# Kernel optimization log

Hardware: AMD Instinct MI355X
Metric: run time of the kernel (lower is better)

## Reference

```python
import jax, jax.numpy as jnp
import numpy as np
from jax.scipy.special import gammaln, xlogy

B, N, DIM, H, DK, DV = 2, 2048, 1536, 8, 64, 64
NRPF = 192  # num_rel_pos_features, already divisible by 6


def get_positional_embed(n, feat):
    # Enformer positional basis: exponential, central-mask, gamma; then sign-antisymmetrized.
    nb = feat // 6  # num basis per class
    d = jnp.arange(-n + 1, n, dtype=jnp.float32)          # [2n-1]
    ad = jnp.abs(d)[:, None]                              # [2n-1, 1]
    # exponential decay features
    max_range = np.log(n) / np.log(2.0)
    half_life = 2.0 ** jnp.linspace(3.0, max_range, nb)
    e = jnp.exp(-np.log(2.0) / half_life * ad)
    # central mask features
    widths = 2.0 ** jnp.arange(1, nb + 1, dtype=jnp.float32) - 1.0
    c = (widths > ad).astype(jnp.float32)
    # gamma pdf features
    std = n / (2.0 * nb)
    mean = jnp.linspace(n / nb, float(n), nb)
    conc = (mean / std) ** 2
    rate = mean / (std ** 2)
    logp = xlogy(conc - 1.0, ad) - rate * ad - (gammaln(conc) - conc * jnp.log(rate))
    p = jnp.exp(logp) + 1e-8
    g = p / jnp.max(p)
    emb = jnp.concatenate([e, c, g], axis=-1)             # [2n-1, feat//2]
    return jnp.concatenate([emb, jnp.sign(d)[:, None] * emb], axis=-1)  # [2n-1, feat]


def relative_shift(x):
    # x: [b, h, i, 2i-1] -> [b, h, i, i]
    b, h, i, j = x.shape
    x = jnp.pad(x, ((0, 0), (0, 0), (0, 0), (1, 0)))      # [b,h,i,j+1]
    x = x.reshape(b, h, j + 1, i)[:, :, 1:, :]            # drop first 'row'
    x = x.reshape(b, h, i, j)
    return x[..., : (j + 2) // 2]                          # keep first i cols


def setup_inputs() -> dict:
    key = jax.random.key(0)
    ks = jax.random.split(key, 9)
    s = 0.02
    return {
        "x": jax.random.normal(ks[0], (B, N, DIM), jnp.float32),
        "Wq": jax.random.normal(ks[1], (DIM, H * DK), jnp.float32) * s,
        "Wk": jax.random.normal(ks[2], (DIM, H * DK), jnp.float32) * s,
        "Wv": jax.random.normal(ks[3], (DIM, H * DV), jnp.float32) * s,
        "Wo": jax.random.normal(ks[4], (H * DV, DIM), jnp.float32) * s,
        "bo": jnp.zeros((DIM,), jnp.float32),
        "Wrel": jax.random.normal(ks[5], (NRPF, H * DK), jnp.float32) * s,
        "rel_content_bias": jax.random.normal(ks[6], (1, H, 1, DK), jnp.float32),
        "rel_pos_bias": jax.random.normal(ks[7], (1, H, 1, DK), jnp.float32),
    }


def reference(x, Wq, Wk, Wv, Wo, bo, Wrel, rel_content_bias, rel_pos_bias):
    b, n, _ = x.shape
    scale = DK ** -0.5
    split = lambda t, d: t.reshape(b, n, H, d).transpose(0, 2, 1, 3)  # b h n d
    q = split(x @ Wq, DK) * scale
    k = split(x @ Wk, DK)
    v = split(x @ Wv, DV)
    content_logits = jnp.einsum('bhid,bhjd->bhij', q + rel_content_bias, k)
    pos = get_positional_embed(n, NRPF) @ Wrel               # [2n-1, H*DK]
    pos = pos.reshape(2 * n - 1, H, DK).transpose(1, 0, 2)   # h j d
    rel_logits = jnp.einsum('bhid,hjd->bhij', q + rel_pos_bias, pos)
    rel_logits = relative_shift(rel_logits)
    attn = jax.nn.softmax(content_logits + rel_logits, axis=-1)
    out = jnp.einsum('bhij,bhjd->bhid', attn, v)
    out = out.transpose(0, 2, 1, 3).reshape(b, n, H * DV)
    return out @ Wo + bo
```

## Files before the change

kernel.cpp:

```cpp
#include <hip/hip_runtime.h>
#include <stdint.h>
#include <cmath>

#define B_    2
#define N_    2048
#define DIM_  1536
#define H_    8
#define NPOS  (2*N_ - 1)
#define NB_   32

typedef __attribute__((ext_vector_type(8))) short short8;
typedef __attribute__((ext_vector_type(4))) float float4v;

struct PosConsts {
    float  inv_hl[32];
    int    widthI[32];
    float  c1[32];
    float  rateF[32];
    double gc[32];
    double maxp;
};

__device__ __forceinline__ float bf2f(unsigned short u) {
    return __uint_as_float(((unsigned int)u) << 16);
}
__device__ __forceinline__ unsigned short f2bf(float f) {
    unsigned int u = __float_as_uint(f);
    u += 0x7FFFu + ((u >> 16) & 1u);
    return (unsigned short)(u >> 16);
}
__device__ __forceinline__ unsigned int cvtpk(float lo, float hi) {
    unsigned int r;
    asm("v_cvt_pk_bf16_f32 %0, %1, %2" : "=v"(r) : "v"(lo), "v"(hi));
    return r;
}
__device__ __forceinline__ unsigned int pack2bf(float lo, float hi) {
    return cvtpk(lo, hi);
}
__device__ __forceinline__ float ldf(const void* p, int isF32, size_t idx) {
    return isF32 ? ((const float*)p)[idx] : bf2f(((const unsigned short*)p)[idx]);
}
__device__ __forceinline__ void gll16(const unsigned short* g, unsigned short* l) {
    __builtin_amdgcn_global_load_lds(
        (const __attribute__((address_space(1))) unsigned int*)g,
        (__attribute__((address_space(3))) unsigned int*)l, 16, 0, 0);
}

constexpr size_t OFF_FLAG = 0;
constexpr size_t OFF_POS  = 256;
constexpr size_t OFF_Q    = OFF_POS + (size_t)H_*4096*64*2;
constexpr size_t OFF_K    = OFF_Q   + (size_t)B_*H_*N_*64*2;
constexpr size_t OFF_V    = OFF_K   + (size_t)B_*H_*N_*64*2;
constexpr size_t OFF_WOT  = OFF_V   + (size_t)B_*H_*N_*64*2;
constexpr size_t OFF_XB   = OFF_WOT + (size_t)DIM_*512*2;
constexpr size_t OFF_AO   = OFF_XB;
constexpr size_t OFF_OP   = OFF_AO + (size_t)4096*512*2;
constexpr size_t OFF_LP   = OFF_OP + (size_t)3*16*32*4096*2;
constexpr size_t OFF_WT   = OFF_XB + (size_t)4096*DIM_*2;
static_assert(OFF_LP + (size_t)3*16*32*64*4 <= OFF_WT + (size_t)3*512*DIM_*2, "ws overflow");

__global__ __launch_bounds__(512) void prep_kernel(PosConsts pc,
                                                   const void* __restrict__ x,
                                                   const void* __restrict__ Wq, const void* __restrict__ Wk,
                                                   const void* __restrict__ Wv, const void* __restrict__ Wo,
                                                   const void* __restrict__ Wrel,
                                                   unsigned int* __restrict__ flags,
                                                   unsigned short* __restrict__ Xb,
                                                   unsigned short* __restrict__ Wt,
                                                   unsigned short* __restrict__ Wot,
                                                   unsigned short* __restrict__ posb) {
    __shared__ __align__(16) char smraw[16 * 192 * 4];
    const int tid = threadIdx.x;
    const int bid = blockIdx.x;

    int* cnt = (int*)smraw;
    int ok = 0;
    if (tid < 256) {
        unsigned short u = ((const unsigned short*)x)[2 * tid];
        int e = (u >> 7) & 0xFF;
        ok = (u == 0) || (e >= 95 && e <= 140);
    }
    cnt[tid] = ok;
    __syncthreads();
    for (int s = 256; s > 0; s >>= 1) {
        if (tid < s) cnt[tid] += cnt[tid + s];
        __syncthreads();
    }
    const int f32 = !(cnt[0] >= 192);
    __syncthreads();
    if (bid == 0 && tid == 0) flags[0] = (unsigned int)f32;

    if (bid < 256) {
        float* eb = (float*)smraw;
        const int j0 = bid * 16;
        const int c  = tid;
        for (int u = c; u < 16 * 96; u += 512) {
            int rr = u / 96, f = u - rr * 96;
            int j = j0 + rr;
            float v = 0.f, sg = 0.f;
            if (j < NPOS) {
                int dd  = j - (N_ - 1);
                int adI = dd < 0 ? -dd : dd;
                float val;
                if (f < 32) {
                    val = exp2f(-(float)adI * pc.inv_hl[f]);
                } else if (f < 64) {
                    val = (adI < pc.widthI[f - 32]) ? 1.f : 0.f;
                } else {
                    int g = f - 64;
                    if (adI == 0) {
                        val = (float)(1e-8 / pc.maxp);
                    } else {
                        double lp = (double)pc.c1[g] * log((double)adI)
                                  - (double)pc.rateF[g] * (double)adI + pc.gc[g];
                        double p = (double)expf((float)lp) + 1e-8;
                        val = (float)(p / pc.maxp);
                    }
                }
                v  = val;
                sg = (dd > 0) ? 1.f : ((dd < 0) ? -1.f : 0.f);
            }
            eb[rr * 192 + f]      = v;
            eb[rr * 192 + 96 + f] = sg * v;
        }
        __syncthreads();
        float acc[16];
#pragma unroll
        for (int rr = 0; rr < 16; ++rr) acc[rr] = 0.f;
        for (int k = 0; k < 192; k += 4) {
            float w0 = ldf(Wrel, f32, (size_t)(k + 0) * 512 + c);
            float w1 = ldf(Wrel, f32, (size_t)(k + 1) * 512 + c);
            float w2 = ldf(Wrel, f32, (size_t)(k + 2) * 512 + c);
            float w3 = ldf(Wrel, f32, (size_t)(k + 3) * 512 + c);
#pragma unroll
            for (int rr = 0; rr < 16; ++rr) {
                float4v e = *reinterpret_cast<const float4v*>(&eb[rr * 192 + k]);
                acc[rr] += e[0] * w0;
                acc[rr] += e[1] * w1;
                acc[rr] += e[2] * w2;
                acc[rr] += e[3] * w3;
            }
        }
        int h = c >> 6, dcol = c & 63;
#pragma unroll
        for (int rr = 0; rr < 16; ++rr) {
            int j = j0 + rr;
            if (j < NPOS)
                posb[((size_t)h * 4096 + j) * 64 + (dcol ^ ((j & 7) << 3))] = f2bf(acc[rr]);
        }
    } else if (bid < 1024) {
        unsigned short (*tile)[66] = (unsigned short(*)[66])smraw;
        const int idx = bid - 256;
        const int z = idx / 192, rem = idx % 192;
        const void* src = z == 0 ? Wq : (z == 1 ? Wk : (z == 2 ? Wv : Wo));
        unsigned short* dst = (z < 3) ? (Wt + (size_t)z * 512 * DIM_) : Wot;
        const int C     = (z < 3) ? 512 : DIM_;
        const int Rrows = (z < 3) ? DIM_ : 512;
        const int xt = C >> 6;
        const int bx = rem % xt, by = rem / xt;
        const int x0 = bx * 64, y0 = by * 64;
        const int tx2 = tid & 63, ty2 = tid >> 6;
#pragma unroll
        for (int i = 0; i < 8; ++i)
            tile[ty2 + i * 8][tx2] = f2bf(ldf(src, f32, (size_t)(y0 + ty2 + i * 8) * C + x0 + tx2));
        __syncthreads();
#pragma unroll
        for (int i = 0; i < 8; ++i)
            dst[(size_t)(x0 + ty2 + i * 8) * Rrows + y0 + tx2] = tile[tx2][ty2 + i * 8];
    } else {
        const int ab = bid - 1024;
        const size_t total = (size_t)4096 * DIM_;
        size_t i = ((size_t)ab * 512 + tid) * 8;
        const size_t stride = (size_t)1024 * 512 * 8;
        if (f32) {
            for (; i < total; i += stride) {
                float4v a = *reinterpret_cast<const float4v*>((const float*)x + i);
                float4v b = *reinterpret_cast<const float4v*>((const float*)x + i + 4);
                uint4 o;
                o.x = pack2bf(a[0], a[1]); o.y = pack2bf(a[2], a[3]);
                o.z = pack2bf(b[0], b[1]); o.w = pack2bf(b[2], b[3]);
                *reinterpret_cast<uint4*>(Xb + i) = o;
            }
        } else {
            for (; i < total; i += stride)
                *reinterpret_cast<uint4*>(Xb + i) =
                    *reinterpret_cast<const uint4*>((const unsigned short*)x + i);
        }
    }
}

__device__ __forceinline__ void gemm64x128_core(const unsigned short* __restrict__ A,
                                                const unsigned short* __restrict__ Bt,
                                                int K, int row0, int col0,
                                                unsigned short* As, unsigned short* Bs,
                                                float4v acc[2][4]) {
    const int tid = threadIdx.x, lane = tid & 63, w = tid >> 6;
    const int l15 = lane & 15, q8 = (lane >> 4) * 8;
    const int mr0 = (w & 1) * 32, nc0 = (w >> 1) * 64;
    const int sr = lane >> 2, sc8 = (lane & 3) * 8;
    for (int k0 = 0; k0 < K; k0 += 32) {
        __syncthreads();
        gll16(&A [(size_t)(row0 + w * 16 + sr) * K + k0 + sc8],      &As[w * 512]);
        gll16(&Bt[(size_t)(col0 + w * 32 + sr) * K + k0 + sc8],      &Bs[w * 1024]);
        gll16(&Bt[(size_t)(col0 + w * 32 + 16 + sr) * K + k0 + sc8], &Bs[w * 1024 + 512]);
        __syncthreads();
        short8 a[2], b[4];
#pragma unroll
        for (int mi = 0; mi < 2; ++mi)
            a[mi] = *reinterpret_cast<const short8*>(&As[(mr0 + mi * 16 + l15) * 32 + q8]);
#pragma unroll
        for (int ni = 0; ni < 4; ++ni)
            b[ni] = *reinterpret_cast<const short8*>(&Bs[(nc0 + ni * 16 + l15) * 32 + q8]);
#pragma unroll
        for (int mi = 0; mi < 2; ++mi)
#pragma unroll
            for (int ni = 0; ni < 4; ++ni)
                acc[mi][ni] = __builtin_amdgcn_mfma_f32_16x16x32_bf16(a[mi], b[ni], acc[mi][ni], 0, 0, 0);
    }
}

__global__ __launch_bounds__(256) void qkv_kernel(const unsigned short* __restrict__ Xb,
                                                  const unsigned short* __restrict__ Wt,
                                                  unsigned short* __restrict__ qbuf,
                                                  unsigned short* __restrict__ kbuf,
                                                  unsigned short* __restrict__ vbuf) {
    __shared__ __align__(16) unsigned short smem[64 * 32 + 128 * 32];
    unsigned short* As = smem;
    unsigned short* Bs = smem + 64 * 32;
    const int row0 = blockIdx.y * 64, col0 = blockIdx.x * 128;
    float4v acc[2][4];
#pragma unroll
    for (int mi = 0; mi < 2; ++mi)
#pragma unroll
        for (int ni = 0; ni < 4; ++ni) acc[mi][ni] = (float4v){0.f, 0.f, 0.f, 0.f};
    gemm64x128_core(Xb, Wt, DIM_, row0, col0, As, Bs, acc);
    __syncthreads();

    const int lane = threadIdx.x & 63, w = threadIdx.x >> 6;
    const int l15 = lane & 15, quad = lane >> 4;
    const int mr0 = (w & 1) * 32, nc0 = (w >> 1) * 64;
    const int n0 = col0 + nc0;
    const int mode = n0 >> 9;
    const int hh = (n0 & 511) >> 6;

    if (mode == 2) {
#pragma unroll
        for (int mi = 0; mi < 2; ++mi)
#pragma unroll
            for (int ni = 0; ni < 4; ++ni) {
                int dd = ni * 16 + l15;
                int mb = row0 + mr0 + mi * 16 + quad * 4;
                int bb = mb >> 11, ii = mb & 2047;
                union { unsigned short us[4]; uint2 u2; } pk;
                unsigned int p0 = cvtpk(acc[mi][ni][0], acc[mi][ni][1]);
                unsigned int p1 = cvtpk(acc[mi][ni][2], acc[mi][ni][3]);
                pk.u2 = (uint2){p0, p1};
                int jb = (ii & ~63) | ((ii & 63) ^ ((dd & 7) << 3));
                *reinterpret_cast<uint2*>(
                    &vbuf[((size_t)(bb * 8 + hh) * 64 + dd) * 2048 + jb]) = pk.u2;
            }
    } else {
        unsigned short* Obuf = (mode == 0) ? qbuf : kbuf;
        const float scale = (mode == 0) ? 0.125f : 1.0f;
        unsigned short* Lw = smem + w * 16 * 72;
        const int r16 = lane >> 2, c4 = (lane & 3) * 16;
#pragma unroll
        for (int mi = 0; mi < 2; ++mi) {
#pragma unroll
            for (int ni = 0; ni < 4; ++ni)
#pragma unroll
                for (int r = 0; r < 4; ++r)
                    Lw[(quad * 4 + r) * 72 + ni * 16 + l15] = f2bf(acc[mi][ni][r] * scale);
            int mb = row0 + mr0 + mi * 16 + r16;
            int bb = mb >> 11, tok = mb & 2047;
            unsigned short* gp = &Obuf[((size_t)(bb * 8 + hh) * N_ + tok) * 64];
            uint4 v0 = *reinterpret_cast<const uint4*>(&Lw[r16 * 72 + c4]);
            uint4 v1 = *reinterpret_cast<const uint4*>(&Lw[r16 * 72 + c4 + 8]);
            int swz2 = (mode == 1) ? ((tok & 7) << 3) : 0;
            *reinterpret_cast<uint4*>(gp + (c4 ^ swz2))       = v0;
            *reinterpret_cast<uint4*>(gp + ((c4 + 8) ^ swz2)) = v1;
        }
    }
}

#define SLD 72
#define RST 68

__device__ __forceinline__ void stage_lin(const unsigned short* __restrict__ g,
                                          unsigned short* s, int tid, int w) {
    gll16(g + tid * 8,        s + w * 512);
    gll16(g + 2048 + tid * 8, s + 2048 + w * 512);
}
__device__ __forceinline__ void stage_vt(const unsigned short* __restrict__ vbase,
                                         int jbase, unsigned short* s, int tid, int w) {
    {
        int L = tid * 8;        int d = L >> 6, cb = L & 63;
        gll16(vbase + (size_t)d * 2048 + jbase + cb, s + w * 512);
    }
    {
        int L = 2048 + tid * 8; int d = L >> 6, cb = L & 63;
        gll16(vbase + (size_t)d * 2048 + jbase + cb, s + 2048 + w * 512);
    }
}

__global__ __launch_bounds__(256) void attn_kernel(const unsigned int* __restrict__ flags,
                                                   const unsigned short* __restrict__ qb,
                                                   const unsigned short* __restrict__ kb,
                                                   const unsigned short* __restrict__ vb,
                                                   const unsigned short* __restrict__ posb,
                                                   const void* __restrict__ rcb,
                                                   const void* __restrict__ rpb,
                                                   unsigned short* __restrict__ ao) {
    __shared__ __align__(16) unsigned short Ks[2][4096];
    __shared__ __align__(16) unsigned short Ps[2][4096];
    __shared__ __align__(16) unsigned short Vt[2][4096];
    __shared__ __align__(16) unsigned short Pp[64 * SLD];
    __shared__ __align__(8)  unsigned short Rb[128 * RST];

    const int f32 = (int)flags[0];
    const int tid = threadIdx.x;
    const int it = blockIdx.x, bh = blockIdx.y;
    const int h = bh & 7, b = bh >> 3;
    const int i0 = it * 64;
    const size_t qoff = (size_t)bh * N_ * 64;
    const size_t poff = (size_t)h * 4096 * 64;
    const unsigned short* vbase = vb + (size_t)bh * 64 * 2048;
    const int lane = tid & 63, w = tid >> 6;
    const int l15 = lane & 15, quad = lane >> 4, q8 = quad * 8;
    const int m0 = w * 16 + quad * 4;
    const int swz = (l15 & 7) << 3;

    short8 afc[2], afr[2];
#pragma unroll
    for (int kc = 0; kc < 2; ++kc) {
        uint4 qv = *reinterpret_cast<const uint4*>(
            &qb[qoff + (size_t)(i0 + w * 16 + l15) * 64 + kc * 32 + q8]);
        unsigned int uu[4] = {qv.x, qv.y, qv.z, qv.w};
        unsigned int cw[4], rw[4];
#pragma unroll
        for (int e = 0; e < 4; ++e) {
            int k = h * 64 + kc * 32 + q8 + 2 * e;
            float lo = __uint_as_float(uu[e] << 16);
            float hi = __uint_as_float(uu[e] & 0xffff0000u);
            cw[e] = pack2bf(lo + ldf(rcb, f32, k), hi + ldf(rcb, f32, k + 1));
            rw[e] = pack2bf(lo + ldf(rpb, f32, k), hi + ldf(rpb, f32, k + 1));
        }
        union { uint4 u; short8 s; } cv, rv2;
        cv.u  = (uint4){cw[0], cw[1], cw[2], cw[3]};
        rv2.u = (uint4){rw[0], rw[1], rw[2], rw[3]};
        afc[kc] = cv.s;
        afr[kc] = rv2.s;
    }

    float4v Oa[4];
#pragma unroll
    for (int nb = 0; nb < 4; ++nb) Oa[nb] = (float4v){0.f, 0.f, 0.f, 0.f};
    float lsum[4] = {0.f, 0.f, 0.f, 0.f};

    const int base0 = 1984 - i0;
    const int NT = 32;
    const int cs0 = base0;

    {
        int r = tid >> 2, c16 = (tid & 3) * 16;
        const uint4* psrc = reinterpret_cast<const uint4*>(&posb[poff + (size_t)(cs0 + r) * 64 + c16]);
        *reinterpret_cast<uint4*>(&Ps[0][r * 64 + c16])     = psrc[0];
        *reinterpret_cast<uint4*>(&Ps[0][r * 64 + c16 + 8]) = psrc[1];
    }
    __syncthreads();
    {
        float4v R[4];
#pragma unroll
        for (int nb = 0; nb < 4; ++nb) R[nb] = (float4v){0.f, 0.f, 0.f, 0.f};
        __builtin_amdgcn_s_setprio(1);
#pragma unroll
        for (int kc = 0; kc < 2; ++kc)
#pragma unroll
            for (int nb = 0; nb < 4; ++nb) {
                short8 pb = *reinterpret_cast<const short8*>(
                    &Ps[0][(nb * 16 + l15) * 64 + ((kc * 32 + q8) ^ swz)]);
                R[nb] = __builtin_amdgcn_mfma_f32_16x16x32_bf16(afr[kc], pb, R[nb], 0, 0, 0);
            }
        __builtin_amdgcn_s_setprio(0);
#pragma unroll
        for (int nb = 0; nb < 4; ++nb) {
            int ta = cs0 + nb * 16 + l15;
            unsigned int pk0 = cvtpk(R[nb][0], R[nb][1]);
            unsigned int pk1 = cvtpk(R[nb][2], R[nb][3]);
            Rb[(size_t)((ta + m0 + 0) & 127) * RST + m0 + 0] = (unsigned short)pk0;
            Rb[(size_t)((ta + m0 + 1) & 127) * RST + m0 + 1] = (unsigned short)(pk0 >> 16);
            Rb[(size_t)((ta + m0 + 2) & 127) * RST + m0 + 2] = (unsigned short)pk1;
            Rb[(size_t)((ta + m0 + 3) & 127) * RST + m0 + 3] = (unsigned short)(pk1 >> 16);
        }
    }
    __syncthreads();

    stage_lin(&kb[qoff], Ks[0], tid, w);
    stage_lin(&posb[poff + (size_t)(cs0 + 64) * 64], Ps[0], tid, w);
    stage_vt(vbase, 0, Vt[0], tid, w);

    for (int u = 0; u < NT; ++u) {
        const int p = u & 1;
        const int j0 = u * 64, basej = base0 + j0;
        __syncthreads();

        if (u + 1 < NT) {
            stage_lin(&kb[qoff + (size_t)(j0 + 64) * 64], Ks[p ^ 1], tid, w);
            stage_lin(&posb[poff + (size_t)(cs0 + (u + 2) * 64) * 64], Ps[p ^ 1], tid, w);
            stage_vt(vbase, j0 + 64, Vt[p ^ 1], tid, w);
        }

        {
            float4v R[4];
#pragma unroll
            for (int nb = 0; nb < 4; ++nb) R[nb] = (float4v){0.f, 0.f, 0.f, 0.f};
            __builtin_amdgcn_s_setprio(1);
#pragma unroll
            for (int kc = 0; kc < 2; ++kc)
#pragma unroll
                for (int nb = 0; nb < 4; ++nb) {
                    short8 pb = *reinterpret_cast<const short8*>(
                        &Ps[p][(nb * 16 + l15) * 64 + ((kc * 32 + q8) ^ swz)]);
                    R[nb] = __builtin_amdgcn_mfma_f32_16x16x32_bf16(afr[kc], pb, R[nb], 0, 0, 0);
                }
            __builtin_amdgcn_s_setprio(0);
            const int tb = basej + 64;
#pragma unroll
            for (int nb = 0; nb < 4; ++nb) {
                int ta = tb + nb * 16 + l15;
                unsigned int pk0 = cvtpk(R[nb][0], R[nb][1]);
                unsigned int pk1 = cvtpk(R[nb][2], R[nb][3]);
                Rb[(size_t)((ta + m0 + 0) & 127) * RST + m0 + 0] = (unsigned short)pk0;
                Rb[(size_t)((ta + m0 + 1) & 127) * RST + m0 + 1] = (unsigned short)(pk0 >> 16);
                Rb[(size_t)((ta + m0 + 2) & 127) * RST + m0 + 2] = (unsigned short)pk1;
                Rb[(size_t)((ta + m0 + 3) & 127) * RST + m0 + 3] = (unsigned short)(pk1 >> 16);
            }
        }

        float4v Sacc[4];
#pragma unroll
        for (int nb = 0; nb < 4; ++nb) Sacc[nb] = (float4v){0.f, 0.f, 0.f, 0.f};
        __builtin_amdgcn_s_setprio(1);
#pragma unroll
        for (int kc = 0; kc < 2; ++kc)
#pragma unroll
            for (int nb = 0; nb < 4; ++nb) {
                short8 kf = *reinterpret_cast<const short8*>(
                    &Ks[p][(nb * 16 + l15) * 64 + ((kc * 32 + q8) ^ swz)]);
                Sacc[nb] = __builtin_amdgcn_mfma_f32_16x16x32_bf16(afc[kc], kf, Sacc[nb], 0, 0, 0);
            }
        __builtin_amdgcn_s_setprio(0);

        float pv4[4][4];
#pragma unroll
        for (int nb = 0; nb < 4; ++nb) {
            const int jl = nb * 16 + l15;
            const int row = (basej + 63 + jl) & 127;
            union { uint2 u2; unsigned short us[4]; } rv;
            rv.u2 = *reinterpret_cast<const uint2*>(&Rb[(size_t)row * RST + m0]);
#pragma unroll
            for (int r = 0; r < 4; ++r) {
                float p2 = __expf(Sacc[nb][r] + bf2f(rv.us[r]));
                pv4[nb][r] = p2;
                lsum[r] += p2;
            }
        }
#pragma unroll
        for (int r = 0; r < 4; ++r) {
            unsigned short* prow = &Pp[(m0 + r) * SLD + l15];
#pragma unroll
            for (int np = 0; np < 2; ++np) {
                unsigned int pk = cvtpk(pv4[2 * np][r], pv4[2 * np + 1][r]);
                prow[(2 * np) * 16]     = (unsigned short)pk;
                prow[(2 * np + 1) * 16] = (unsigned short)(pk >> 16);
            }
        }

        __builtin_amdgcn_s_setprio(1);
#pragma unroll
        for (int kc = 0; kc < 2; ++kc) {
            short8 pf = *reinterpret_cast<const short8*>(&Pp[(w * 16 + l15) * SLD + kc * 32 + q8]);
#pragma unroll
            for (int nb = 0; nb < 4; ++nb) {
                short8 vf = *reinterpret_cast<const short8*>(
                    &Vt[p][(nb * 16 + l15) * 64 + ((kc * 32 + q8) ^ swz)]);
                Oa[nb] = __builtin_amdgcn_mfma_f32_16x16x32_bf16(pf, vf, Oa[nb], 0, 0, 0);
            }
        }
        __builtin_amdgcn_s_setprio(0);
    }

#pragma unroll
    for (int r = 0; r < 4; ++r) {
#pragma unroll
        for (int off = 1; off < 16; off <<= 1) lsum[r] += __shfl_xor(lsum[r], off);
        lsum[r] = 1.0f / lsum[r];
    }
#pragma unroll
    for (int nb = 0; nb < 4; ++nb) {
        unsigned int pk0 = cvtpk(Oa[nb][0] * lsum[0], Oa[nb][1] * lsum[1]);
        unsigned int pk1 = cvtpk(Oa[nb][2] * lsum[2], Oa[nb][3] * lsum[3]);
        unsigned short* prow = &Pp[m0 * SLD + nb * 16 + l15];
        prow[0 * SLD] = (unsigned short)pk0;
        prow[1 * SLD] = (unsigned short)(pk0 >> 16);
        prow[2 * SLD] = (unsigned short)pk1;
        prow[3 * SLD] = (unsigned short)(pk1 >> 16);
    }
    {
        const int rr2 = w * 16 + (lane >> 2), cc2 = (lane & 3) * 16;
        uint4 o0 = *reinterpret_cast<const uint4*>(&Pp[rr2 * SLD + cc2]);
        uint4 o1 = *reinterpret_cast<const uint4*>(&Pp[rr2 * SLD + cc2 + 8]);
        unsigned short* dst = &ao[((size_t)(b * N_ + i0 + rr2)) * 512 + h * 64 + cc2];
        *reinterpret_cast<uint4*>(dst)     = o0;
        *reinterpret_cast<uint4*>(dst + 8) = o1;
    }
}

__global__ __launch_bounds__(256) void outproj_kernel(const unsigned int* __restrict__ flags,
                                                      const unsigned short* __restrict__ AO,
                                                      const unsigned short* __restrict__ Wot,
                                                      const void* __restrict__ bo,
                                                      void* __restrict__ out) {
    __shared__ __align__(16) unsigned short As[64 * 32];
    __shared__ __align__(16) unsigned short Bs[128 * 32];
    const int f32 = (int)flags[0];
    const int row0 = blockIdx.y * 64, col0 = blockIdx.x * 128;
    float4v acc[2][4];
#pragma unroll
    for (int mi = 0; mi < 2; ++mi)
#pragma unroll
        for (int ni = 0; ni < 4; ++ni) acc[mi][ni] = (float4v){0.f, 0.f, 0.f, 0.f};
    gemm64x128_core(AO, Wot, 512, row0, col0, As, Bs, acc);
    const int lane = threadIdx.x & 63, w = threadIdx.x >> 6;
    const int l15 = lane & 15, quad = lane >> 4;
    const int mr0 = (w & 1) * 32, nc0 = (w >> 1) * 64;
#pragma unroll
    for (int mi = 0; mi < 2; ++mi)
#pragma unroll
        for (int ni = 0; ni < 4; ++ni) {
            int n = col0 + nc0 + ni * 16 + l15;
            float bias = ldf(bo, f32, n);
#pragma unroll
            for (int r = 0; r < 4; ++r) {
                int m = row0 + mr0 + mi * 16 + quad * 4 + r;
                float v = acc[mi][ni][r] + bias;
                if (f32) ((float*)out)[(size_t)m * DIM_ + n] = v;
                else     ((unsigned short*)out)[(size_t)m * DIM_ + n] = f2bf(v);
            }
        }
}

extern "C" void kernel_launch(void* const* d_in, const int* in_sizes, int n_in,
                              void* d_out, int out_size, void* d_ws, size_t ws_size,
                              hipStream_t stream) {
    const void* x    = d_in[0];
    const void* Wq   = d_in[1];
    const void* Wk   = d_in[2];
    const void* Wv   = d_in[3];
    const void* Wo   = d_in[4];
    const void* bo   = d_in[5];
    const void* Wrel = d_in[6];
    const void* rcb  = d_in[7];
    const void* rpb  = d_in[8];

    char* ws = (char*)d_ws;
    unsigned int*   flags = (unsigned int*)(ws + OFF_FLAG);
    unsigned short* posb  = (unsigned short*)(ws + OFF_POS);
    unsigned short* qbuf  = (unsigned short*)(ws + OFF_Q);
    unsigned short* kbuf  = (unsigned short*)(ws + OFF_K);
    unsigned short* vbuf  = (unsigned short*)(ws + OFF_V);
    unsigned short* Wot   = (unsigned short*)(ws + OFF_WOT);
    unsigned short* Xb    = (unsigned short*)(ws + OFF_XB);
    unsigned short* ao    = (unsigned short*)(ws + OFF_AO);
    unsigned short* Wt    = (unsigned short*)(ws + OFF_WT);

    PosConsts pc;
    double maxp = 0.0;
    for (int g = 0; g < NB_; ++g) {
        double mean = 64.0 * (g + 1);
        double conc = (mean / 32.0) * (mean / 32.0);
        double rate = mean / 1024.0;
        double lgc  = std::lgamma(conc);
        double clr  = conc * std::log(rate);
        for (int ad = 1; ad < N_; ++ad) {
            double lp = (conc - 1.0) * std::log((double)ad) - rate * (double)ad - lgc + clr;
            double p  = std::exp(lp) + 1e-8;
            if (p > maxp) maxp = p;
        }
        pc.c1[g]    = (float)(conc - 1.0);
        pc.rateF[g] = (float)rate;
        pc.gc[g]    = -lgc + clr;
    }
    pc.maxp = maxp;
    const double max_range = std::log((double)N_) / std::log(2.0);
    for (int f = 0; f < 32; ++f) {
        double t = 3.0 + (double)f * (max_range - 3.0) / 31.0;
        pc.inv_hl[f] = (float)std::exp2(-t);
        int e = f + 1;
        pc.widthI[f] = (e >= 12) ? 0x7FFFFFFF : ((1 << e) - 1);
    }

    prep_kernel<<<dim3(2048), dim3(512), 0, stream>>>(pc, x, Wq, Wk, Wv, Wo, Wrel,
                                                      flags, Xb, Wt, Wot, posb);
    qkv_kernel<<<dim3(12, 64), dim3(256), 0, stream>>>(Xb, Wt, qbuf, kbuf, vbuf);
    attn_kernel<<<dim3(32, 16), dim3(256), 0, stream>>>(flags, qbuf, kbuf, vbuf, posb, rcb, rpb, ao);
    outproj_kernel<<<dim3(12, 64), dim3(256), 0, stream>>>(flags, ao, Wot, bo, d_out);
}
```

Measured before the change: 247.8 us.

## Split attention key tiles across waves and keep P in registers for PV

Reorganizes the attention kernel so each wave owns a 16-key slice of every 64-key tile and computes transposed scores for all 64 queries. The probabilities stay in registers and feed a 16x16x16 MFMA directly, which removes the Pp shared-memory round trip. The V swizzle changes to match the new read pattern, and the per-wave partial outputs and row sums are reduced through shared memory at the end. The cost is more accumulator registers (16 output tiles per wave), a serialized cross-wave reduction, and the weaker 16x16x16 MFMA. The launch bound now requests two blocks per SM.

Result: faster. 240.4 us (median of 2 runs) (-3.0%).

```diff
diff --git a/kernel.cpp b/kernel.cpp
--- a/kernel.cpp
+++ b/kernel.cpp
@@ -10,6 +10,7 @@
 #define NB_   32
 
 typedef __attribute__((ext_vector_type(8))) short short8;
+typedef __attribute__((ext_vector_type(4))) short short4v;
 typedef __attribute__((ext_vector_type(4))) float float4v;
 
 struct PosConsts {
@@ -255,7 +256,7 @@
                 unsigned int p0 = cvtpk(acc[mi][ni][0], acc[mi][ni][1]);
                 unsigned int p1 = cvtpk(acc[mi][ni][2], acc[mi][ni][3]);
                 pk.u2 = (uint2){p0, p1};
-                int jb = (ii & ~63) | ((ii & 63) ^ ((dd & 7) << 3));
+                int jb = (ii & ~63) | ((ii & 63) ^ ((dd & 7) << 2));
                 *reinterpret_cast<uint2*>(
                     &vbuf[((size_t)(bb * 8 + hh) * 64 + dd) * 2048 + jb]) = pk.u2;
             }
@@ -283,7 +284,6 @@
     }
 }
 
-#define SLD 72
 #define RST 68
 
 __device__ __forceinline__ void stage_lin(const unsigned short* __restrict__ g,
@@ -303,19 +303,16 @@
     }
 }
 
-__global__ __launch_bounds__(256) void attn_kernel(const unsigned int* __restrict__ flags,
-                                                   const unsigned short* __restrict__ qb,
-                                                   const unsigned short* __restrict__ kb,
-                                                   const unsigned short* __restrict__ vb,
-                                                   const unsigned short* __restrict__ posb,
-                                                   const void* __restrict__ rcb,
-                                                   const void* __restrict__ rpb,
-                                                   unsigned short* __restrict__ ao) {
-    __shared__ __align__(16) unsigned short Ks[2][4096];
-    __shared__ __align__(16) unsigned short Ps[2][4096];
-    __shared__ __align__(16) unsigned short Vt[2][4096];
-    __shared__ __align__(16) unsigned short Pp[64 * SLD];
-    __shared__ __align__(8)  unsigned short Rb[128 * RST];
+__global__ __launch_bounds__(256, 2) void attn_kernel(const unsigned int* __restrict__ flags,
+                                                      const unsigned short* __restrict__ qb,
+                                                      const unsigned short* __restrict__ kb,
+                                                      const unsigned short* __restrict__ vb,
+                                                      const unsigned short* __restrict__ posb,
+                                                      const void* __restrict__ rcb,
+                                                      const void* __restrict__ rpb,
+                                                      unsigned short* __restrict__ ao) {
+    __shared__ __align__(16) unsigned short SM[33280];
+    unsigned short* Rb = SM + 24576;
 
     const int f32 = (int)flags[0];
     const int tid = threadIdx.x;
@@ -326,193 +323,213 @@
     const size_t poff = (size_t)h * 4096 * 64;
     const unsigned short* vbase = vb + (size_t)bh * 64 * 2048;
     const int lane = tid & 63, w = tid >> 6;
-    const int l15 = lane & 15, quad = lane >> 4, q8 = quad * 8;
-    const int m0 = w * 16 + quad * 4;
+    const int l15 = lane & 15, quad = lane >> 4, q8 = quad * 8, q4 = quad * 4;
     const int swz = (l15 & 7) << 3;
-
-    short8 afc[2], afr[2];
-#pragma unroll
-    for (int kc = 0; kc < 2; ++kc) {
-        uint4 qv = *reinterpret_cast<const uint4*>(
-            &qb[qoff + (size_t)(i0 + w * 16 + l15) * 64 + kc * 32 + q8]);
-        unsigned int uu[4] = {qv.x, qv.y, qv.z, qv.w};
-        unsigned int cw[4], rw[4];
-#pragma unroll
-        for (int e = 0; e < 4; ++e) {
-            int k = h * 64 + kc * 32 + q8 + 2 * e;
-            float lo = __uint_as_float(uu[e] << 16);
-            float hi = __uint_as_float(uu[e] & 0xffff0000u);
-            cw[e] = pack2bf(lo + ldf(rcb, f32, k), hi + ldf(rcb, f32, k + 1));
-            rw[e] = pack2bf(lo + ldf(rpb, f32, k), hi + ldf(rpb, f32, k + 1));
-        }
-        union { uint4 u; short8 s; } cv, rv2;
-        cv.u  = (uint4){cw[0], cw[1], cw[2], cw[3]};
-        rv2.u = (uint4){rw[0], rw[1], rw[2], rw[3]};
-        afc[kc] = cv.s;
-        afr[kc] = rv2.s;
-    }
-
-    float4v Oa[4];
-#pragma unroll
-    for (int nb = 0; nb < 4; ++nb) Oa[nb] = (float4v){0.f, 0.f, 0.f, 0.f};
+    const int vsw = (l15 & 7) << 2;
+
+    short8 afc[4][2], afr[4][2];
+#pragma unroll
+    for (int mb = 0; mb < 4; ++mb)
+#pragma unroll
+        for (int kc = 0; kc < 2; ++kc) {
+            uint4 qv = *reinterpret_cast<const uint4*>(
+                &qb[qoff + (size_t)(i0 + mb * 16 + l15) * 64 + kc * 32 + q8]);
+            unsigned int uu[4] = {qv.x, qv.y, qv.z, qv.w};
+            unsigned int cw[4], rw[4];
+#pragma unroll
+            for (int e = 0; e < 4; ++e) {
+                int k = h * 64 + kc * 32 + q8 + 2 * e;
+                float lo = __uint_as_float(uu[e] << 16);
+                float hi = __uint_as_float(uu[e] & 0xffff0000u);
+                cw[e] = pack2bf(lo + ldf(rcb, f32, k), hi + ldf(rcb, f32, k + 1));
+                rw[e] = pack2bf(lo + ldf(rpb, f32, k), hi + ldf(rpb, f32, k + 1));
+            }
+            union { uint4 u; short8 s; } cv, rv2;
+            cv.u  = (uint4){cw[0], cw[1], cw[2], cw[3]};
+            rv2.u = (uint4){rw[0], rw[1], rw[2], rw[3]};
+            afc[mb][kc] = cv.s;
+            afr[mb][kc] = rv2.s;
+        }
+
+    float4v Oa[4][4];
+#pragma unroll
+    for (int db = 0; db < 4; ++db)
+#pragma unroll
+        for (int mb = 0; mb < 4; ++mb) Oa[db][mb] = (float4v){0.f, 0.f, 0.f, 0.f};
     float lsum[4] = {0.f, 0.f, 0.f, 0.f};
 
     const int base0 = 1984 - i0;
     const int NT = 32;
     const int cs0 = base0;
 
+    unsigned short* Ks0 = SM;
+    unsigned short* Ps0 = SM + 8192;
+    unsigned short* Vt0 = SM + 16384;
+
     {
         int r = tid >> 2, c16 = (tid & 3) * 16;
         const uint4* psrc = reinterpret_cast<const uint4*>(&posb[poff + (size_t)(cs0 + r) * 64 + c16]);
-        *reinterpret_cast<uint4*>(&Ps[0][r * 64 + c16])     = psrc[0];
-        *reinterpret_cast<uint4*>(&Ps[0][r * 64 + c16 + 8]) = psrc[1];
+        *reinterpret_cast<uint4*>(&Ps0[r * 64 + c16])     = psrc[0];
+        *reinterpret_cast<uint4*>(&Ps0[r * 64 + c16 + 8]) = psrc[1];
     }
     __syncthreads();
     {
         float4v R[4];
 #pragma unroll
-        for (int nb = 0; nb < 4; ++nb) R[nb] = (float4v){0.f, 0.f, 0.f, 0.f};
+        for (int mb = 0; mb < 4; ++mb) R[mb] = (float4v){0.f, 0.f, 0.f, 0.f};
         __builtin_amdgcn_s_setprio(1);
 #pragma unroll
-        for (int kc = 0; kc < 2; ++kc)
-#pragma unroll
-            for (int nb = 0; nb < 4; ++nb) {
-                short8 pb = *reinterpret_cast<const short8*>(
-                    &Ps[0][(nb * 16 + l15) * 64 + ((kc * 32 + q8) ^ swz)]);
-                R[nb] = __builtin_amdgcn_mfma_f32_16x16x32_bf16(afr[kc], pb, R[nb], 0, 0, 0);
-            }
+        for (int kc = 0; kc < 2; ++kc) {
+            short8 pb = *reinterpret_cast<const short8*>(
+                &Ps0[(w * 16 + l15) * 64 + ((kc * 32 + q8) ^ swz)]);
+#pragma unroll
+            for (int mb = 0; mb < 4; ++mb)
+                R[mb] = __builtin_amdgcn_mfma_f32_16x16x32_bf16(pb, afr[mb][kc], R[mb], 0, 0, 0);
+        }
         __builtin_amdgcn_s_setprio(0);
 #pragma unroll
-        for (int nb = 0; nb < 4; ++nb) {
-            int ta = cs0 + nb * 16 + l15;
-            unsigned int pk0 = cvtpk(R[nb][0], R[nb][1]);
-            unsigned int pk1 = cvtpk(R[nb][2], R[nb][3]);
-            Rb[(size_t)((ta + m0 + 0) & 127) * RST + m0 + 0] = (unsigned short)pk0;
-            Rb[(size_t)((ta + m0 + 1) & 127) * RST + m0 + 1] = (unsigned short)(pk0 >> 16);
-            Rb[(size_t)((ta + m0 + 2) & 127) * RST + m0 + 2] = (unsigned short)pk1;
-            Rb[(size_t)((ta + m0 + 3) & 127) * RST + m0 + 3] = (unsigned short)(pk1 >> 16);
+        for (int mb = 0; mb < 4; ++mb) {
+            const int col = mb * 16 + l15;
+            const int R0 = cs0 + w * 16 + q4 + col;
+            unsigned int pk0 = cvtpk(R[mb][0], R[mb][1]);
+            unsigned int pk1 = cvtpk(R[mb][2], R[mb][3]);
+            Rb[((R0 + 0) & 127) * RST + col] = (unsigned short)pk0;
+            Rb[((R0 + 1) & 127) * RST + col] = (unsigned short)(pk0 >> 16);
+            Rb[((R0 + 2) & 127) * RST + col] = (unsigned short)pk1;
+            Rb[((R0 + 3) & 127) * RST + col] = (unsigned short)(pk1 >> 16);
         }
     }
     __syncthreads();
 
-    stage_lin(&kb[qoff], Ks[0], tid, w);
-    stage_lin(&posb[poff + (size_t)(cs0 + 64) * 64], Ps[0], tid, w);
-    stage_vt(vbase, 0, Vt[0], tid, w);
+    stage_lin(&kb[qoff], Ks0, tid, w);
+    stage_lin(&posb[poff + (size_t)(cs0 + 64) * 64], Ps0, tid, w);
+    stage_vt(vbase, 0, Vt0, tid, w);
 
     for (int u = 0; u < NT; ++u) {
         const int p = u & 1;
         const int j0 = u * 64, basej = base0 + j0;
+        unsigned short* Ksp = SM + p * 4096;
+        unsigned short* Psp = SM + 8192 + p * 4096;
+        unsigned short* Vtp = SM + 16384 + p * 4096;
+        __syncthreads();
+
+        float4v St[4], R[4];
+#pragma unroll
+        for (int mb = 0; mb < 4; ++mb) {
+            St[mb] = (float4v){0.f, 0.f, 0.f, 0.f};
+            R[mb]  = (float4v){0.f, 0.f, 0.f, 0.f};
+        }
+        __builtin_amdgcn_s_setprio(1);
+#pragma unroll
+        for (int kc = 0; kc < 2; ++kc) {
+            short8 kf = *reinterpret_cast<const short8*>(
+                &Ksp[(w * 16 + l15) * 64 + ((kc * 32 + q8) ^ swz)]);
+            short8 pb = *reinterpret_cast<const short8*>(
+                &Psp[(w * 16 + l15) * 64 + ((kc * 32 + q8) ^ swz)]);
+#pragma unroll
+            for (int mb = 0; mb < 4; ++mb) {
+                St[mb] = __builtin_amdgcn_mfma_f32_16x16x32_bf16(kf, afc[mb][kc], St[mb], 0, 0, 0);
+                R[mb]  = __builtin_amdgcn_mfma_f32_16x16x32_bf16(pb, afr[mb][kc], R[mb], 0, 0, 0);
+            }
+        }
+        __builtin_amdgcn_s_setprio(0);
+
+        {
+            const int tb = basej + 64;
+#pragma unroll
+            for (int mb = 0; mb < 4; ++mb) {
+                const int col = mb * 16 + l15;
+                const int R0 = tb + w * 16 + q4 + col;
+                unsigned int pk0 = cvtpk(R[mb][0], R[mb][1]);
+                unsigned int pk1 = cvtpk(R[mb][2], R[mb][3]);
+                Rb[((R0 + 0) & 127) * RST + col] = (unsigned short)pk0;
+                Rb[((R0 + 1) & 127) * RST + col] = (unsigned short)(pk0 >> 16);
+                Rb[((R0 + 2) & 127) * RST + col] = (unsigned short)pk1;
+                Rb[((R0 + 3) & 127) * RST + col] = (unsigned short)(pk1 >> 16);
+            }
+        }
         __syncthreads();
 
         if (u + 1 < NT) {
-            stage_lin(&kb[qoff + (size_t)(j0 + 64) * 64], Ks[p ^ 1], tid, w);
-            stage_lin(&posb[poff + (size_t)(cs0 + (u + 2) * 64) * 64], Ps[p ^ 1], tid, w);
-            stage_vt(vbase, j0 + 64, Vt[p ^ 1], tid, w);
-        }
-
-        {
-            float4v R[4];
-#pragma unroll
-            for (int nb = 0; nb < 4; ++nb) R[nb] = (float4v){0.f, 0.f, 0.f, 0.f};
-            __builtin_amdgcn_s_setprio(1);
-#pragma unroll
-            for (int kc = 0; kc < 2; ++kc)
-#pragma unroll
-                for (int nb = 0; nb < 4; ++nb) {
-                    short8 pb = *reinterpret_cast<const short8*>(
-                        &Ps[p][(nb * 16 + l15) * 64 + ((kc * 32 + q8) ^ swz)]);
-                    R[nb] = __builtin_amdgcn_mfma_f32_16x16x32_bf16(afr[kc], pb, R[nb], 0, 0, 0);
-                }
-            __builtin_amdgcn_s_setprio(0);
-            const int tb = basej + 64;
-#pragma unroll
-            for (int nb = 0; nb < 4; ++nb) {
-                int ta = tb + nb * 16 + l15;
-                unsigned int pk0 = cvtpk(R[nb][0], R[nb][1]);
-                unsigned int pk1 = cvtpk(R[nb][2], R[nb][3]);
-                Rb[(size_t)((ta + m0 + 0) & 127) * RST + m0 + 0] = (unsigned short)pk0;
-                Rb[(size_t)((ta + m0 + 1) & 127) * RST + m0 + 1] = (unsigned short)(pk0 >> 16);
-                Rb[(size_t)((ta + m0 + 2) & 127) * RST + m0 + 2] = (unsigned short)pk1;
-                Rb[(size_t)((ta + m0 + 3) & 127) * RST + m0 + 3] = (unsigned short)(pk1 >> 16);
-            }
-        }
-
-        float4v Sacc[4];
-#pragma unroll
-        for (int nb = 0; nb < 4; ++nb) Sacc[nb] = (float4v){0.f, 0.f, 0.f, 0.f};
+            stage_lin(&kb[qoff + (size_t)(j0 + 64) * 64], SM + (p ^ 1) * 4096, tid, w);
+            stage_lin(&posb[poff + (size_t)(cs0 + (u + 2) * 64) * 64], SM + 8192 + (p ^ 1) * 4096, tid, w);
+            stage_vt(vbase, j0 + 64, SM + 16384 + (p ^ 1) * 4096, tid, w);
+        }
+
+        short4v pb16[4];
+        const int G0 = basej + 63 + w * 16 + q4;
+#pragma unroll
+        for (int mb = 0; mb < 4; ++mb) {
+            const int col = mb * 16 + l15;
+            float pv[4];
+#pragma unroll
+            for (int r = 0; r < 4; ++r) {
+                float rel = bf2f(Rb[((G0 + r) & 127) * RST + col]);
+                float p2 = __expf(St[mb][r] + rel);
+                lsum[mb] += p2;
+                pv[r] = p2;
+            }
+            union { unsigned int u2[2]; short4v s; } pk;
+            pk.u2[0] = cvtpk(pv[0], pv[1]);
+            pk.u2[1] = cvtpk(pv[2], pv[3]);
+            pb16[mb] = pk.s;
+        }
+
         __builtin_amdgcn_s_setprio(1);
 #pragma unroll
-        for (int kc = 0; kc < 2; ++kc)
-#pragma unroll
-            for (int nb = 0; nb < 4; ++nb) {
-                short8 kf = *reinterpret_cast<const short8*>(
-                    &Ks[p][(nb * 16 + l15) * 64 + ((kc * 32 + q8) ^ swz)]);
-                Sacc[nb] = __builtin_amdgcn_mfma_f32_16x16x32_bf16(afc[kc], kf, Sacc[nb], 0, 0, 0);
-            }
+        for (int db = 0; db < 4; ++db) {
+            short4v vf = *reinterpret_cast<const short4v*>(
+                &Vtp[(db * 16 + l15) * 64 + ((w * 16 + q4) ^ vsw)]);
+#pragma unroll
+            for (int mb = 0; mb < 4; ++mb)
+                Oa[db][mb] = __builtin_amdgcn_mfma_f32_16x16x16bf16_1k(vf, pb16[mb], Oa[db][mb], 0, 0, 0);
+        }
         __builtin_amdgcn_s_setprio(0);
-
-        float pv4[4][4];
-#pragma unroll
-        for (int nb = 0; nb < 4; ++nb) {
-            const int jl = nb * 16 + l15;
-            const int row = (basej + 63 + jl) & 127;
-            union { uint2 u2; unsigned short us[4]; } rv;
-            rv.u2 = *reinterpret_cast<const uint2*>(&Rb[(size_t)row * RST + m0]);
-#pragma unroll
-            for (int r = 0; r < 4; ++r) {
-                float p2 = __expf(Sacc[nb][r] + bf2f(rv.us[r]));
-                pv4[nb][r] = p2;
-                lsum[r] += p2;
-            }
-        }
-#pragma unroll
-        for (int r = 0; r < 4; ++r) {
-            unsigned short* prow = &Pp[(m0 + r) * SLD + l15];
-#pragma unroll
-            for (int np = 0; np < 2; ++np) {
-                unsigned int pk = cvtpk(pv4[2 * np][r], pv4[2 * np + 1][r]);
-                prow[(2 * np) * 16]     = (unsigned short)pk;
-                prow[(2 * np + 1) * 16] = (unsigned short)(pk >> 16);
-            }
-        }
-
-        __builtin_amdgcn_s_setprio(1);
-#pragma unroll
-        for (int kc = 0; kc < 2; ++kc) {
-            short8 pf = *reinterpret_cast<const short8*>(&Pp[(w * 16 + l15) * SLD + kc * 32 + q8]);
-#pragma unroll
-            for (int nb = 0; nb < 4; ++nb) {
-                short8 vf = *reinterpret_cast<const short8*>(
-                    &Vt[p][(nb * 16 + l15) * 64 + ((kc * 32 + q8) ^ swz)]);
-                Oa[nb] = __builtin_amdgcn_mfma_f32_16x16x32_bf16(pf, vf, Oa[nb], 0, 0, 0);
-            }
-        }
-        __builtin_amdgcn_s_setprio(0);
-    }
-
-#pragma unroll
-    for (int r = 0; r < 4; ++r) {
-#pragma unroll
-        for (int off = 1; off < 16; off <<= 1) lsum[r] += __shfl_xor(lsum[r], off);
-        lsum[r] = 1.0f / lsum[r];
-    }
-#pragma unroll
-    for (int nb = 0; nb < 4; ++nb) {
-        unsigned int pk0 = cvtpk(Oa[nb][0] * lsum[0], Oa[nb][1] * lsum[1]);
-        unsigned int pk1 = cvtpk(Oa[nb][2] * lsum[2], Oa[nb][3] * lsum[3]);
-        unsigned short* prow = &Pp[m0 * SLD + nb * 16 + l15];
-        prow[0 * SLD] = (unsigned short)pk0;
-        prow[1 * SLD] = (unsigned short)(pk0 >> 16);
-        prow[2 * SLD] = (unsigned short)pk1;
-        prow[3 * SLD] = (unsigned short)(pk1 >> 16);
-    }
+    }
+
+#pragma unroll
+    for (int mb = 0; mb < 4; ++mb) {
+        lsum[mb] += __shfl_xor(lsum[mb], 16);
+        lsum[mb] += __shfl_xor(lsum[mb], 32);
+    }
+
+    __syncthreads();
+    float* Of = (float*)SM;
+    float* Ls = (float*)(SM + 8320);
+#pragma unroll
+    for (int ww = 0; ww < 4; ++ww) {
+        if (w == ww) {
+            if (quad == 0) {
+#pragma unroll
+                for (int mb = 0; mb < 4; ++mb) Ls[ww * 64 + mb * 16 + l15] = lsum[mb];
+            }
+#pragma unroll
+            for (int db = 0; db < 4; ++db)
+#pragma unroll
+                for (int mb = 0; mb < 4; ++mb)
+#pragma unroll
+                    for (int r = 0; r < 4; ++r) {
+                        float* slot = &Of[(db * 16 + q4 + r) * 65 + mb * 16 + l15];
+                        if (ww == 0) *slot = Oa[db][mb][r];
+                        else         *slot += Oa[db][mb][r];
+                    }
+        }
+        __syncthreads();
+    }
+
     {
-        const int rr2 = w * 16 + (lane >> 2), cc2 = (lane & 3) * 16;
-        uint4 o0 = *reinterpret_cast<const uint4*>(&Pp[rr2 * SLD + cc2]);
-        uint4 o1 = *reinterpret_cast<const uint4*>(&Pp[rr2 * SLD + cc2 + 8]);
-        unsigned short* dst = &ao[((size_t)(b * N_ + i0 + rr2)) * 512 + h * 64 + cc2];
-        *reinterpret_cast<uint4*>(dst)     = o0;
-        *reinterpret_cast<uint4*>(dst + 8) = o1;
+        const int m = tid >> 2, c0 = (tid & 3) * 16;
+        float inv = 1.0f / (Ls[m] + Ls[64 + m] + Ls[128 + m] + Ls[192 + m]);
+        unsigned int ou[8];
+#pragma unroll
+        for (int e = 0; e < 8; ++e) {
+            float lo = Of[(c0 + 2 * e) * 65 + m] * inv;
+            float hi = Of[(c0 + 2 * e + 1) * 65 + m] * inv;
+            ou[e] = cvtpk(lo, hi);
+        }
+        unsigned short* dst = &ao[((size_t)(b * N_ + i0 + m)) * 512 + h * 64 + c0];
+        *reinterpret_cast<uint4*>(dst)     = (uint4){ou[0], ou[1], ou[2], ou[3]};
+        *reinterpret_cast<uint4*>(dst + 8) = (uint4){ou[4], ou[5], ou[6], ou[7]};
     }
 }
 
```
